# Performance work log

Hardware: AMD Instinct MI355X
Metric: run time of the kernel (lower is better)

The kernel has to match this reference:

```python
import jax, jax.numpy as jnp
import numpy as np


def setup_inputs() -> dict:
    key = jax.random.key(0)
    k1, k2, k3 = jax.random.split(key, 3)
    B, C, Q, E = 32, 2048, 128, 200
    x_contexts = jax.random.normal(k1, (B, C, E), dtype=jnp.float32)
    x_questions = jax.random.normal(k2, (B, Q, E), dtype=jnp.float32)
    # weight of nn.Linear(3E, 1, bias=False), flattened to (3E,)
    w_sim = jax.random.normal(k3, (3 * E,), dtype=jnp.float32) * (1.0 / np.sqrt(3 * E))
    return {"x_contexts": x_contexts, "x_questions": x_questions, "w_sim": w_sim}


def reference(x_contexts, x_questions, w_sim):
    # x_contexts: [B,C,E], x_questions: [B,Q,E], w_sim: [3E]
    E = x_contexts.shape[-1]
    w1, w2, w3 = w_sim[:E], w_sim[E:2 * E], w_sim[2 * E:]
    # Trilinear similarity S[b,c,q] = w1.c + w2.q + w3.(c*q), decomposed so the
    # [B,C,Q,3E] tensor of the original expand+cat+linear is never materialized.
    s_c = jnp.einsum('bce,e->bc', x_contexts, w1)              # [B,C]
    s_q = jnp.einsum('bqe,e->bq', x_questions, w2)             # [B,Q]
    s_cq = jnp.einsum('bce,bqe->bcq', x_contexts * w3, x_questions)  # [B,C,Q]
    S = s_cq + s_c[:, :, None] + s_q[:, None, :]               # [B,C,Q]

    # Context-to-question: row softmax over Q, then attend over questions.
    c2q = jnp.einsum('bcq,bqe->bce', jax.nn.softmax(S, axis=-1), x_questions)

    # Question-to-context: max over Q, softmax over C, attend over contexts.
    q2c_w = jax.nn.softmax(jnp.max(S, axis=-1), axis=-1)       # [B,C]
    q2c = jnp.einsum('bc,bce->be', q2c_w, x_contexts)          # [B,E]
    q2c = q2c[:, None, :]                                      # broadcast to [B,C,E]

    return jnp.concatenate(
        [x_contexts, c2q, x_contexts * c2q, x_contexts * q2c], axis=-1)  # [B,C,4E]
```

## Files before the change

### kernel.cpp

```cpp
#include <hip/hip_runtime.h>

#define B_ 32
#define C_ 2048
#define Q_ 128
#define E_ 200
#define TB 32

typedef __attribute__((ext_vector_type(4))) float f32x4;

__global__ __launch_bounds__(256) void xqt_kernel(const float* __restrict__ xq,
                                                  float* __restrict__ xqT) {
    __shared__ float tl[32][33];
    const int blk = blockIdx.x;
    const int b  = blk / 28;
    const int r  = blk - b * 28;
    const int qt = r / 7, et = r - (r / 7) * 7;
    const int q0 = qt * 32, e0 = et * 32;
    const int tx = threadIdx.x & 31, ty = threadIdx.x >> 5;
    #pragma unroll
    for (int i = 0; i < 4; ++i) {
        const int q = q0 + ty + 8 * i, e = e0 + tx;
        if (e < E_) tl[ty + 8 * i][tx] = xq[((size_t)b * Q_ + q) * E_ + e];
    }
    __syncthreads();
    #pragma unroll
    for (int i = 0; i < 4; ++i) {
        const int e = e0 + ty + 8 * i, q = q0 + tx;
        if (e < E_) xqT[((size_t)b * E_ + e) * Q_ + q] = tl[tx][ty + 8 * i];
    }
}

__global__ __launch_bounds__(128) void sq_kernel(const float* __restrict__ xqT,
                                                 const float* __restrict__ w,
                                                 float* __restrict__ sq) {
    const int b = blockIdx.x, q = threadIdx.x;
    const float* base = xqT + (size_t)b * E_ * Q_ + q;
    float a = 0.f;
    #pragma unroll 8
    for (int e = 0; e < E_; ++e) a = fmaf(base[e * Q_], w[E_ + e], a);
    sq[b * Q_ + q] = a;
}

__global__ __launch_bounds__(256) void row2_kernel(const float* __restrict__ xc_g,
                                                   const float* __restrict__ xq_g,
                                                   const float* __restrict__ xqT_g,
                                                   const float* __restrict__ w_g,
                                                   const float* __restrict__ sq_g,
                                                   float* __restrict__ m_g,
                                                   float* __restrict__ out) {
    __shared__ float buf[TB][E_];
    __shared__ float sc_l[TB];

    const int t = threadIdx.x;
    const int blk = blockIdx.x;
    const int x   = blk & 7;
    const int g   = blk >> 3;
    const int b   = x * 4 + (g >> 6);
    const int tile = g & 63;
    const int bc0 = b * C_ + tile * TB;

    {
        const int r  = t >> 3;
        const int k  = t & 7;
        const int e0 = k * 25;
        const float* xc_row = xc_g + (size_t)(bc0 + r) * E_;
        float p1 = 0.f;
        #pragma unroll
        for (int i = 0; i < 25; ++i) {
            const int e = e0 + i;
            const float v = xc_row[e];
            buf[r][e] = v * w_g[2 * E_ + e];
            p1 = fmaf(v, w_g[e], p1);
        }
        p1 += __shfl_xor(p1, 1);
        p1 += __shfl_xor(p1, 2);
        p1 += __shfl_xor(p1, 4);
        if (k == 0) sc_l[r] = p1;
    }
    __syncthreads();

    const int qg = t & 31;
    const int cg = t >> 5;
    const int c4 = cg * 4;
    const int q4 = qg * 4;

    f32x4 acc[4] = {};
    const float* xqT_b = xqT_g + (size_t)b * E_ * Q_;
    #pragma unroll 2
    for (int e = 0; e < E_; e += 4) {
        const f32x4 x0 = *(const f32x4*)&xqT_b[(e + 0) * Q_ + q4];
        const f32x4 x1 = *(const f32x4*)&xqT_b[(e + 1) * Q_ + q4];
        const f32x4 x2 = *(const f32x4*)&xqT_b[(e + 2) * Q_ + q4];
        const f32x4 x3 = *(const f32x4*)&xqT_b[(e + 3) * Q_ + q4];
        #pragma unroll
        for (int ci = 0; ci < 4; ++ci) {
            const f32x4 a = *(const f32x4*)&buf[c4 + ci][e];
            acc[ci] += a.x * x0 + a.y * x1 + a.z * x2 + a.w * x3;
        }
    }
    __syncthreads();

    const f32x4 sqv = *(const f32x4*)&sq_g[b * Q_ + q4];
    float mx[4], sm[4];
    #pragma unroll
    for (int ci = 0; ci < 4; ++ci) {
        acc[ci] += sc_l[c4 + ci] + sqv;
        mx[ci] = fmaxf(fmaxf(acc[ci].x, acc[ci].y), fmaxf(acc[ci].z, acc[ci].w));
    }
    #pragma unroll
    for (int off = 16; off; off >>= 1) {
        #pragma unroll
        for (int ci = 0; ci < 4; ++ci) mx[ci] = fmaxf(mx[ci], __shfl_xor(mx[ci], off));
    }
    if (qg == 0) {
        #pragma unroll
        for (int ci = 0; ci < 4; ++ci) m_g[bc0 + c4 + ci] = mx[ci];
    }
    #pragma unroll
    for (int ci = 0; ci < 4; ++ci) {
        f32x4 p;
        p.x = __expf(acc[ci].x - mx[ci]);
        p.y = __expf(acc[ci].y - mx[ci]);
        p.z = __expf(acc[ci].z - mx[ci]);
        p.w = __expf(acc[ci].w - mx[ci]);
        acc[ci] = p;
        sm[ci] = (p.x + p.y) + (p.z + p.w);
    }
    #pragma unroll
    for (int off = 16; off; off >>= 1) {
        #pragma unroll
        for (int ci = 0; ci < 4; ++ci) sm[ci] += __shfl_xor(sm[ci], off);
    }
    #pragma unroll
    for (int ci = 0; ci < 4; ++ci) {
        acc[ci] *= (1.f / sm[ci]);
        *(f32x4*)&buf[c4 + ci][q4] = acc[ci];
    }
    __syncthreads();

    const float* xq_b = xq_g + (size_t)b * Q_ * E_;
    #pragma unroll
    for (int pass = 0; pass < 2; ++pass) {
        const int e4 = pass * 128 + q4;
        if (e4 < E_) {
            f32x4 o[4] = {};
            for (int q = 0; q < Q_; q += 4) {
                const f32x4 xv0 = *(const f32x4*)&xq_b[(q + 0) * E_ + e4];
                const f32x4 xv1 = *(const f32x4*)&xq_b[(q + 1) * E_ + e4];
                const f32x4 xv2 = *(const f32x4*)&xq_b[(q + 2) * E_ + e4];
                const f32x4 xv3 = *(const f32x4*)&xq_b[(q + 3) * E_ + e4];
                #pragma unroll
                for (int ci = 0; ci < 4; ++ci) {
                    const f32x4 p = *(const f32x4*)&buf[c4 + ci][q];
                    o[ci] += p.x * xv0 + p.y * xv1 + p.z * xv2 + p.w * xv3;
                }
            }
            #pragma unroll
            for (int ci = 0; ci < 4; ++ci) {
                const size_t row = (size_t)(bc0 + c4 + ci);
                const f32x4 xcv = *(const f32x4*)&xc_g[row * E_ + e4];
                float* orow = out + row * (4 * E_);
                *(f32x4*)&orow[e4]          = xcv;
                *(f32x4*)&orow[E_ + e4]     = o[ci];
                *(f32x4*)&orow[2 * E_ + e4] = xcv * o[ci];
            }
        }
    }
}

__global__ __launch_bounds__(256) void stats_kernel(const float* __restrict__ m_g,
                                                    float* __restrict__ bstat) {
    __shared__ float red[4];
    const int b = blockIdx.x, t = threadIdx.x;
    float mx = -3.4e38f;
    for (int c = t; c < C_; c += 256) mx = fmaxf(mx, m_g[b * C_ + c]);
    #pragma unroll
    for (int off = 32; off; off >>= 1) mx = fmaxf(mx, __shfl_xor(mx, off));
    if ((t & 63) == 0) red[t >> 6] = mx;
    __syncthreads();
    mx = fmaxf(fmaxf(red[0], red[1]), fmaxf(red[2], red[3]));
    __syncthreads();
    float sum = 0.f;
    for (int c = t; c < C_; c += 256) sum += __expf(m_g[b * C_ + c] - mx);
    #pragma unroll
    for (int off = 32; off; off >>= 1) sum += __shfl_xor(sum, off);
    if ((t & 63) == 0) red[t >> 6] = sum;
    __syncthreads();
    if (t == 0) {
        bstat[b]      = mx;
        bstat[B_ + b] = red[0] + red[1] + red[2] + red[3];
    }
}

__global__ __launch_bounds__(256) void q2c_partial(const float* __restrict__ xc_g,
                                                   const float* __restrict__ m_g,
                                                   const float* __restrict__ bstat,
                                                   float* __restrict__ part) {
    __shared__ float wl[128];
    const int blk = blockIdx.x;
    const int x = blk & 7, u = blk >> 3;
    const int b = x * 4 + (u >> 4), g = u & 15;
    const int t = threadIdx.x;
    const float mx  = bstat[b];
    const float inv = 1.f / bstat[B_ + b];
    if (t < 128) wl[t] = __expf(m_g[b * C_ + g * 128 + t] - mx) * inv;
    __syncthreads();
    if (t < E_) {
        float acc = 0.f;
        const float* base = xc_g + ((size_t)(b * C_ + g * 128)) * E_ + t;
        #pragma unroll 8
        for (int c = 0; c < 128; ++c) acc = fmaf(wl[c], base[(size_t)c * E_], acc);
        part[(size_t)(b * 16 + g) * E_ + t] = acc;
    }
}

__global__ __launch_bounds__(256) void q2c_reduce(const float* __restrict__ part,
                                                  float* __restrict__ q2c) {
    const int b = blockIdx.x, t = threadIdx.x;
    if (t < E_) {
        float a = 0.f;
        #pragma unroll
        for (int g = 0; g < 16; ++g) a += part[(size_t)(b * 16 + g) * E_ + t];
        q2c[b * E_ + t] = a;
    }
}

__global__ __launch_bounds__(256) void out4_kernel(const float* __restrict__ xc_g,
                                                   const float* __restrict__ q2c,
                                                   float* __restrict__ out) {
    const unsigned int idx = blockIdx.x * 256u + threadIdx.x;
    const unsigned int n = idx * 4u;
    const unsigned int e = n % E_;
    const unsigned int row = n / E_;
    const unsigned int b = row / C_;
    const f32x4 xcv = *(const f32x4*)&xc_g[n];
    const f32x4 qv  = *(const f32x4*)&q2c[b * E_ + e];
    *(f32x4*)&out[(size_t)row * (4 * E_) + 3 * E_ + e] = xcv * qv;
}

extern "C" void kernel_launch(void* const* d_in, const int* in_sizes, int n_in,
                              void* d_out, int out_size, void* d_ws, size_t ws_size,
                              hipStream_t stream) {
    const float* xc = (const float*)d_in[0];
    const float* xq = (const float*)d_in[1];
    const float* w  = (const float*)d_in[2];
    for (int i = 0; i < n_in; ++i) {
        if      (in_sizes[i] == B_ * C_ * E_) xc = (const float*)d_in[i];
        else if (in_sizes[i] == B_ * Q_ * E_) xq = (const float*)d_in[i];
        else if (in_sizes[i] == 3 * E_)       w  = (const float*)d_in[i];
    }
    float* out = (float*)d_out;

    float* ws    = (float*)d_ws;
    float* sq    = ws;
    float* m     = sq + B_ * Q_;
    float* bstat = m + B_ * C_;
    float* q2c   = bstat + 2 * B_;
    float* xqT   = q2c + B_ * E_;
    float* part  = xqT;

    xqt_kernel  <<<B_ * 28,         256, 0, stream>>>(xq, xqT);
    sq_kernel   <<<B_,              128, 0, stream>>>(xqT, w, sq);
    row2_kernel <<<B_ * (C_ / TB),  256, 0, stream>>>(xc, xq, xqT, w, sq, m, out);
    stats_kernel<<<B_,              256, 0, stream>>>(m, bstat);
    q2c_partial <<<B_ * 16,         256, 0, stream>>>(xc, m, bstat, part);
    q2c_reduce  <<<B_,              256, 0, stream>>>(part, q2c);
    out4_kernel <<<(B_ * C_ * E_ / 4) / 256, 256, 0, stream>>>(xc, q2c, out);
}
```

Before: 455.3 us.

## Fold softmax stats into q2c partials with online rescaling, parallelize sq

Removes the separate stats kernel by having each q2c partial block compute a local max and exp-sum over 64 contexts. The reduce kernel then merges the partials with online-softmax rescaling. The sq kernel now uses one wave per question row with vector loads and a shuffle reduction, and row2 uses separate shared buffers so one barrier can be dropped. Block-to-batch mapping in row2 is simplified, which drops the earlier XCD-aware interleaving and may change cache locality.

```diff
diff --git a/kernel.cpp b/kernel.cpp
--- a/kernel.cpp
+++ b/kernel.cpp
@@ -30,15 +30,21 @@
     }
 }
 
-__global__ __launch_bounds__(128) void sq_kernel(const float* __restrict__ xqT,
+__global__ __launch_bounds__(256) void sq_kernel(const float* __restrict__ xq,
                                                  const float* __restrict__ w,
                                                  float* __restrict__ sq) {
-    const int b = blockIdx.x, q = threadIdx.x;
-    const float* base = xqT + (size_t)b * E_ * Q_ + q;
+    const int wave = blockIdx.x * 4 + (threadIdx.x >> 6);
+    const int lane = threadIdx.x & 63;
+    const float* row = xq + (size_t)wave * E_;
     float a = 0.f;
-    #pragma unroll 8
-    for (int e = 0; e < E_; ++e) a = fmaf(base[e * Q_], w[E_ + e], a);
-    sq[b * Q_ + q] = a;
+    if (lane < 50) {
+        const f32x4 v  = *(const f32x4*)&row[lane * 4];
+        const f32x4 wv = *(const f32x4*)&w[E_ + lane * 4];
+        a = (v.x * wv.x + v.y * wv.y) + (v.z * wv.z + v.w * wv.w);
+    }
+    #pragma unroll
+    for (int off = 32; off; off >>= 1) a += __shfl_xor(a, off);
+    if (lane == 0) sq[wave] = a;
 }
 
 __global__ __launch_bounds__(256) void row2_kernel(const float* __restrict__ xc_g,
@@ -48,16 +54,14 @@
                                                    const float* __restrict__ sq_g,
                                                    float* __restrict__ m_g,
                                                    float* __restrict__ out) {
-    __shared__ float buf[TB][E_];
+    __shared__ float scw3_l[TB][E_];
+    __shared__ float P_l[TB][Q_];
     __shared__ float sc_l[TB];
 
-    const int t = threadIdx.x;
-    const int blk = blockIdx.x;
-    const int x   = blk & 7;
-    const int g   = blk >> 3;
-    const int b   = x * 4 + (g >> 6);
-    const int tile = g & 63;
-    const int bc0 = b * C_ + tile * TB;
+    const int t    = threadIdx.x;
+    const int b    = blockIdx.x >> 6;
+    const int tile = blockIdx.x & 63;
+    const int bc0  = b * C_ + tile * TB;
 
     {
         const int r  = t >> 3;
@@ -69,7 +73,7 @@
         for (int i = 0; i < 25; ++i) {
             const int e = e0 + i;
             const float v = xc_row[e];
-            buf[r][e] = v * w_g[2 * E_ + e];
+            scw3_l[r][e] = v * w_g[2 * E_ + e];
             p1 = fmaf(v, w_g[e], p1);
         }
         p1 += __shfl_xor(p1, 1);
@@ -86,7 +90,6 @@
 
     f32x4 acc[4] = {};
     const float* xqT_b = xqT_g + (size_t)b * E_ * Q_;
-    #pragma unroll 2
     for (int e = 0; e < E_; e += 4) {
         const f32x4 x0 = *(const f32x4*)&xqT_b[(e + 0) * Q_ + q4];
         const f32x4 x1 = *(const f32x4*)&xqT_b[(e + 1) * Q_ + q4];
@@ -94,11 +97,10 @@
         const f32x4 x3 = *(const f32x4*)&xqT_b[(e + 3) * Q_ + q4];
         #pragma unroll
         for (int ci = 0; ci < 4; ++ci) {
-            const f32x4 a = *(const f32x4*)&buf[c4 + ci][e];
+            const f32x4 a = *(const f32x4*)&scw3_l[c4 + ci][e];
             acc[ci] += a.x * x0 + a.y * x1 + a.z * x2 + a.w * x3;
         }
     }
-    __syncthreads();
 
     const f32x4 sqv = *(const f32x4*)&sq_g[b * Q_ + q4];
     float mx[4], sm[4];
@@ -134,7 +136,7 @@
     #pragma unroll
     for (int ci = 0; ci < 4; ++ci) {
         acc[ci] *= (1.f / sm[ci]);
-        *(f32x4*)&buf[c4 + ci][q4] = acc[ci];
+        *(f32x4*)&P_l[c4 + ci][q4] = acc[ci];
     }
     __syncthreads();
 
@@ -151,7 +153,7 @@
                 const f32x4 xv3 = *(const f32x4*)&xq_b[(q + 3) * E_ + e4];
                 #pragma unroll
                 for (int ci = 0; ci < 4; ++ci) {
-                    const f32x4 p = *(const f32x4*)&buf[c4 + ci][q];
+                    const f32x4 p = *(const f32x4*)&P_l[c4 + ci][q];
                     o[ci] += p.x * xv0 + p.y * xv1 + p.z * xv2 + p.w * xv3;
                 }
             }
@@ -168,60 +170,67 @@
     }
 }
 
-__global__ __launch_bounds__(256) void stats_kernel(const float* __restrict__ m_g,
-                                                    float* __restrict__ bstat) {
-    __shared__ float red[4];
-    const int b = blockIdx.x, t = threadIdx.x;
-    float mx = -3.4e38f;
-    for (int c = t; c < C_; c += 256) mx = fmaxf(mx, m_g[b * C_ + c]);
-    #pragma unroll
-    for (int off = 32; off; off >>= 1) mx = fmaxf(mx, __shfl_xor(mx, off));
-    if ((t & 63) == 0) red[t >> 6] = mx;
-    __syncthreads();
-    mx = fmaxf(fmaxf(red[0], red[1]), fmaxf(red[2], red[3]));
-    __syncthreads();
-    float sum = 0.f;
-    for (int c = t; c < C_; c += 256) sum += __expf(m_g[b * C_ + c] - mx);
-    #pragma unroll
-    for (int off = 32; off; off >>= 1) sum += __shfl_xor(sum, off);
-    if ((t & 63) == 0) red[t >> 6] = sum;
-    __syncthreads();
-    if (t == 0) {
-        bstat[b]      = mx;
-        bstat[B_ + b] = red[0] + red[1] + red[2] + red[3];
-    }
-}
-
 __global__ __launch_bounds__(256) void q2c_partial(const float* __restrict__ xc_g,
                                                    const float* __restrict__ m_g,
-                                                   const float* __restrict__ bstat,
-                                                   float* __restrict__ part) {
-    __shared__ float wl[128];
+                                                   float* __restrict__ part,
+                                                   float* __restrict__ pmax,
+                                                   float* __restrict__ psum) {
+    __shared__ float wl[64];
+    __shared__ float red;
     const int blk = blockIdx.x;
-    const int x = blk & 7, u = blk >> 3;
-    const int b = x * 4 + (u >> 4), g = u & 15;
+    const int b = blk >> 5, g = blk & 31;
     const int t = threadIdx.x;
-    const float mx  = bstat[b];
-    const float inv = 1.f / bstat[B_ + b];
-    if (t < 128) wl[t] = __expf(m_g[b * C_ + g * 128 + t] - mx) * inv;
-    __syncthreads();
+    const int c0 = g * 64;
+
+    const float v = (t < 64) ? m_g[b * C_ + c0 + t] : -3.4e38f;
+    if (t < 64) {
+        float mxl = v;
+        #pragma unroll
+        for (int off = 32; off; off >>= 1) mxl = fmaxf(mxl, __shfl_xor(mxl, off));
+        const float e = __expf(v - mxl);
+        wl[t] = e;
+        float s = e;
+        #pragma unroll
+        for (int off = 32; off; off >>= 1) s += __shfl_xor(s, off);
+        if (t == 0) { pmax[blk] = mxl; psum[blk] = s; red = mxl; }
+    }
+    __syncthreads();
+
     if (t < E_) {
         float acc = 0.f;
-        const float* base = xc_g + ((size_t)(b * C_ + g * 128)) * E_ + t;
+        const float* base = xc_g + ((size_t)(b * C_ + c0)) * E_ + t;
         #pragma unroll 8
-        for (int c = 0; c < 128; ++c) acc = fmaf(wl[c], base[(size_t)c * E_], acc);
-        part[(size_t)(b * 16 + g) * E_ + t] = acc;
+        for (int c = 0; c < 64; ++c) acc = fmaf(wl[c], base[(size_t)c * E_], acc);
+        part[(size_t)blk * E_ + t] = acc;
     }
 }
 
 __global__ __launch_bounds__(256) void q2c_reduce(const float* __restrict__ part,
+                                                  const float* __restrict__ pmax,
+                                                  const float* __restrict__ psum,
                                                   float* __restrict__ q2c) {
+    __shared__ float sc[32];
+    __shared__ float inv_total;
     const int b = blockIdx.x, t = threadIdx.x;
+    if (t < 64) {
+        const float pm = (t < 32) ? pmax[b * 32 + t] : -3.4e38f;
+        float M = pm;
+        #pragma unroll
+        for (int off = 32; off; off >>= 1) M = fmaxf(M, __shfl_xor(M, off));
+        const float s = (t < 32) ? __expf(pm - M) : 0.f;
+        float tot = (t < 32) ? psum[b * 32 + t] * s : 0.f;
+        #pragma unroll
+        for (int off = 32; off; off >>= 1) tot += __shfl_xor(tot, off);
+        if (t < 32) sc[t] = s;
+        if (t == 0) inv_total = 1.f / tot;
+    }
+    __syncthreads();
     if (t < E_) {
         float a = 0.f;
         #pragma unroll
-        for (int g = 0; g < 16; ++g) a += part[(size_t)(b * 16 + g) * E_ + t];
-        q2c[b * E_ + t] = a;
+        for (int g = 0; g < 32; ++g)
+            a = fmaf(part[(size_t)(b * 32 + g) * E_ + t], sc[g], a);
+        q2c[b * E_ + t] = a * inv_total;
     }
 }
 
@@ -254,16 +263,16 @@
     float* ws    = (float*)d_ws;
     float* sq    = ws;
     float* m     = sq + B_ * Q_;
-    float* bstat = m + B_ * C_;
-    float* q2c   = bstat + 2 * B_;
+    float* q2c   = m + B_ * C_;
     float* xqT   = q2c + B_ * E_;
     float* part  = xqT;
-
-    xqt_kernel  <<<B_ * 28,         256, 0, stream>>>(xq, xqT);
-    sq_kernel   <<<B_,              128, 0, stream>>>(xqT, w, sq);
-    row2_kernel <<<B_ * (C_ / TB),  256, 0, stream>>>(xc, xq, xqT, w, sq, m, out);
-    stats_kernel<<<B_,              256, 0, stream>>>(m, bstat);
-    q2c_partial <<<B_ * 16,         256, 0, stream>>>(xc, m, bstat, part);
-    q2c_reduce  <<<B_,              256, 0, stream>>>(part, q2c);
+    float* pmax  = xqT + 262144;
+    float* psum  = xqT + 262144 + 2048;
+
+    xqt_kernel  <<<B_ * 28,            256, 0, stream>>>(xq, xqT);
+    sq_kernel   <<<B_ * Q_ / 4,        256, 0, stream>>>(xq, w, sq);
+    row2_kernel <<<B_ * (C_ / TB),     256, 0, stream>>>(xc, xq, xqT, w, sq, m, out);
+    q2c_partial <<<B_ * 32,            256, 0, stream>>>(xc, m, part, pmax, psum);
+    q2c_reduce  <<<B_,                 256, 0, stream>>>(part, pmax, psum, q2c);
     out4_kernel <<<(B_ * C_ * E_ / 4) / 256, 256, 0, stream>>>(xc, q2c, out);
 }
```

Result: faster. 407.6 us (-10.5%).
